# Performance work log

Hardware: AMD Instinct MI355X
Metric: run time of the kernel (lower is better)

## Reference

```python
import jax, jax.numpy as jnp
import numpy as np

N_HEADS = 32
N_KV_HEADS = 8
HEAD_DIM = 128
DIM = 4096
ROPE_THETA = 500000.0
BSZ, SEQLEN = 4, 1024


def _rope(t, cos, sin):
    # t: [B,S,H,hd]; cos/sin: [S,hd//2]
    te = t[..., 0::2]
    to = t[..., 1::2]
    c = cos[None, :, None, :]
    s = sin[None, :, None, :]
    out = jnp.stack([te * c - to * s, te * s + to * c], axis=-1)
    return out.reshape(t.shape)


def setup_inputs() -> dict:
    key = jax.random.key(0)
    ks = jax.random.split(key, 8)
    scale = 1.0 / np.sqrt(DIM)
    x = jax.random.normal(ks[0], (BSZ, SEQLEN, DIM), dtype=jnp.float32)
    wq = jax.random.normal(ks[1], (DIM, N_HEADS * HEAD_DIM), dtype=jnp.float32) * scale
    wk = jax.random.normal(ks[2], (DIM, N_KV_HEADS * HEAD_DIM), dtype=jnp.float32) * scale
    wv = jax.random.normal(ks[3], (DIM, N_KV_HEADS * HEAD_DIM), dtype=jnp.float32) * scale
    wo = jax.random.normal(ks[4], (N_HEADS * HEAD_DIM, DIM), dtype=jnp.float32) * scale
    # rotary tables: freqs_cis[s, j] = exp(i * s * theta^(-2j/hd))
    inv_freq = 1.0 / (ROPE_THETA ** (np.arange(0, HEAD_DIM, 2, dtype=np.float32) / HEAD_DIM))
    ang = np.outer(np.arange(SEQLEN, dtype=np.float32), inv_freq)
    freqs_cos = jnp.asarray(np.cos(ang), dtype=jnp.float32)
    freqs_sin = jnp.asarray(np.sin(ang), dtype=jnp.float32)
    # additive causal mask: 0 on/below diag, -inf above
    causal_mask = jnp.triu(jnp.full((SEQLEN, SEQLEN), -jnp.inf, dtype=jnp.float32), k=1)
    return {"x": x, "wq": wq, "wk": wk, "wv": wv, "wo": wo,
            "freqs_cos": freqs_cos, "freqs_sin": freqs_sin,
            "causal_mask": causal_mask, "fixed_point_iter": 0, "start_pos": 0}


def reference(x, wq, wk, wv, wo, freqs_cos, freqs_sin, causal_mask, fixed_point_iter, start_pos):
    B, S, _ = x.shape
    n_rep = N_HEADS // N_KV_HEADS
    xq = (x @ wq).reshape(B, S, N_HEADS, HEAD_DIM)
    xk = (x @ wk).reshape(B, S, N_KV_HEADS, HEAD_DIM)
    xv = (x @ wv).reshape(B, S, N_KV_HEADS, HEAD_DIM)
    xq = _rope(xq, freqs_cos, freqs_sin)
    xk = _rope(xk, freqs_cos, freqs_sin)
    # start_pos == 0 prefill: cache slice [:start_pos+S] equals freshly written xk/xv
    keys = jnp.repeat(xk, n_rep, axis=2)    # [B,S,H,hd]
    values = jnp.repeat(xv, n_rep, axis=2)
    scores = jnp.einsum('bqhd,bkhd->bhqk', xq, keys) / np.sqrt(HEAD_DIM)
    scores = scores + causal_mask  # broadcast [S,S]
    probs = jax.nn.softmax(scores.astype(jnp.float32), axis=-1).astype(xq.dtype)
    out = jnp.einsum('bhqk,bkhd->bqhd', probs, values)
    out = out.reshape(B, S, N_HEADS * HEAD_DIM)
    return out @ wo
```

## Files before the change

### kernel.cpp

```cpp
#include <hip/hip_runtime.h>

#define BSZ_  4
#define SEQ_  1024
#define NH_   32
#define NKVH_ 8
#define HD_   128
#define DIM_  4096
#define NTOK_ (BSZ_ * SEQ_)
#define QKVW_ 6144

typedef float  floatx4  __attribute__((ext_vector_type(4)));
typedef float  floatx16 __attribute__((ext_vector_type(16)));
typedef __bf16 bf16x8   __attribute__((ext_vector_type(8)));
typedef unsigned short ushortx8 __attribute__((ext_vector_type(8)));

__device__ __forceinline__ float fast_exp2(float x) {
  return __builtin_amdgcn_exp2f(x);
}

__device__ __forceinline__ unsigned short f2bf_bits(float f) {
  unsigned int u = __float_as_uint(f);
  u += 0x7FFFu + ((u >> 16) & 1u);
  return (unsigned short)(u >> 16);
}
__device__ __forceinline__ unsigned int pack_bf2_rne(float lo, float hi_) {
  return (unsigned int)f2bf_bits(lo) | ((unsigned int)f2bf_bits(hi_) << 16);
}
__device__ __forceinline__ unsigned int pack_bf2_trunc(float lo, float hi_) {
  return __builtin_amdgcn_perm(__float_as_uint(hi_), __float_as_uint(lo), 0x07060302u);
}

__device__ __forceinline__ void gld16(const void* g, void* l) {
  __builtin_amdgcn_global_load_lds(
      (const __attribute__((address_space(1))) void*)g,
      (__attribute__((address_space(3))) void*)l, 16, 0, 0);
}

__global__ __launch_bounds__(256)
void xconv(const float* __restrict__ X, unsigned short* __restrict__ XB)
{
  size_t i = ((size_t)blockIdx.x * 256 + threadIdx.x) * 4;
  float4 v = *(const float4*)&X[i];
  ushort4 o;
  o.x = f2bf_bits(v.x); o.y = f2bf_bits(v.y);
  o.z = f2bf_bits(v.z); o.w = f2bf_bits(v.w);
  *(ushort4*)&XB[i] = o;
}

__global__ __launch_bounds__(256)
void wtrans(const float* __restrict__ W, unsigned short* __restrict__ WT,
            int K, int N)
{
  __shared__ unsigned short T[32][36];
  const int k0 = blockIdx.y * 32, n0 = blockIdx.x * 32;
  const int t = threadIdx.x;
  {
    int kr = t >> 3, nc = (t & 7) * 4;
    float4 v = *(const float4*)&W[(size_t)(k0 + kr) * N + n0 + nc];
    T[kr][nc + 0] = f2bf_bits(v.x);
    T[kr][nc + 1] = f2bf_bits(v.y);
    T[kr][nc + 2] = f2bf_bits(v.z);
    T[kr][nc + 3] = f2bf_bits(v.w);
  }
  __syncthreads();
  {
    int nr = t >> 3, kc = (t & 7) * 4;
    ushort4 o;
    o.x = T[kc + 0][nr]; o.y = T[kc + 1][nr];
    o.z = T[kc + 2][nr]; o.w = T[kc + 3][nr];
    *(ushort4*)&WT[(size_t)(n0 + nr) * K + k0 + kc] = o;
  }
}

__global__ __launch_bounds__(256)
void vtrans2(const unsigned short* __restrict__ qkv, unsigned short* __restrict__ VT)
{
  __shared__ unsigned short T[32][36];
  const int bh = blockIdx.z;
  const int s0 = blockIdx.x * 32, d0 = blockIdx.y * 32;
  const int b = bh >> 3, kvh = bh & 7;
  const int t = threadIdx.x;
  {
    int sr = t >> 3, dc = (t & 7) * 4;
    ushort4 v = *(const ushort4*)&qkv[(size_t)(b * SEQ_ + s0 + sr) * QKVW_ + 5120 + kvh * HD_ + d0 + dc];
    T[sr][dc + 0] = v.x; T[sr][dc + 1] = v.y;
    T[sr][dc + 2] = v.z; T[sr][dc + 3] = v.w;
  }
  __syncthreads();
  {
    int dr = t >> 3, sc = (t & 7) * 4;
    ushort4 o;
    o.x = T[sc + 0][dr]; o.y = T[sc + 1][dr];
    o.z = T[sc + 2][dr]; o.w = T[sc + 3][dr];
    *(ushort4*)&VT[((size_t)bh * HD_ + d0 + dr) * SEQ_ + s0 + sc] = o;
  }
}

__global__ __launch_bounds__(256)
void rope2(unsigned int* __restrict__ t, const float* __restrict__ cosf,
           const float* __restrict__ sinf, int shift, int stride_u32, int base_u32)
{
  int idx = blockIdx.x * 256 + threadIdx.x;
  int tok = idx >> shift;
  int rem = idx & ((1 << shift) - 1);
  int d2  = idx & 63;
  int pos = tok & (SEQ_ - 1);
  unsigned int* p = &t[(size_t)tok * stride_u32 + base_u32 + rem];
  unsigned int pv = *p;
  float xe = __uint_as_float(pv << 16);
  float xo = __uint_as_float(pv & 0xFFFF0000u);
  float cv = cosf[pos * 64 + d2];
  float sv = sinf[pos * 64 + d2];
  float oe = xe * cv - xo * sv;
  float oo = xe * sv + xo * cv;
  *p = pack_bf2_rne(oe, oo);
}

template<bool OUT_BF16>
__global__ __launch_bounds__(512, 2)
void gemm_bt8(const unsigned short* __restrict__ A,
              const unsigned short* __restrict__ B,
              void* __restrict__ Cout, int M, int N, int K)
{
  __shared__ __align__(16) unsigned short As[4][256][32];
  __shared__ __align__(16) unsigned short Bs[4][256][32];

  const int tid  = threadIdx.x;
  const int w    = tid >> 6;
  const int lane = tid & 63;
  const int l16  = lane & 15;
  const int quad = lane >> 4;
  const int wr   = w >> 2;
  const int wc   = w & 3;

  int wg = blockIdx.x;
  const int q8 = gridDim.x >> 3;
  wg = (wg & 7) * q8 + (wg >> 3);
  const int nbx = N >> 8;
  const int bm = (wg / nbx) * 256;
  const int bn = (wg % nbx) * 256;

  const int srow     = w * 16 + (lane >> 2);
  const int cs_stage = (lane & 3) ^ ((srow >> 1) & 3);
  const int ntiles   = K >> 5;

  auto stageA = [&](int kt, int buf) {
#pragma unroll
    for (int r = 0; r < 2; r++)
      gld16(&A[(size_t)(bm + r * 128 + srow) * K + (kt << 5) + cs_stage * 8],
            (char*)&As[buf][0][0] + r * 8192 + w * 1024);
  };
  auto stageB = [&](int kt, int buf) {
#pragma unroll
    for (int r = 0; r < 2; r++)
      gld16(&B[(size_t)(bn + r * 128 + srow) * K + (kt << 5) + cs_stage * 8],
            (char*)&Bs[buf][0][0] + r * 8192 + w * 1024);
  };

  floatx4 acc[8][4];
#pragma unroll
  for (int i = 0; i < 8; i++)
#pragma unroll
    for (int j = 0; j < 4; j++) acc[i][j] = (floatx4){0.f, 0.f, 0.f, 0.f};

  const int sfrag = (l16 >> 1) & 3;
  const int cfr   = quad ^ sfrag;

#pragma unroll
  for (int t = 0; t < 3; t++) { stageA(t, t); stageB(t, t); }
  asm volatile("s_waitcnt vmcnt(8)" ::: "memory");
  __builtin_amdgcn_s_barrier();

  for (int t = 0; t < ntiles; t++) {
    const int buf  = t & 3;
    const int pbuf = (t + 3) & 3;
    const int pk   = (t + 3 < ntiles) ? (t + 3) : 0;
    const unsigned short* Ab = &As[buf][0][0];
    const unsigned short* Bb = &Bs[buf][0][0];

    bf16x8 bfr[4], af0[4], af1[4];
#pragma unroll
    for (int nj = 0; nj < 4; nj++)
      bfr[nj] = *(const bf16x8*)&Bb[(wc * 64 + nj * 16 + l16) * 32 + cfr * 8];
#pragma unroll
    for (int i = 0; i < 4; i++)
      af0[i] = *(const bf16x8*)&Ab[(wr * 128 + i * 16 + l16) * 32 + cfr * 8];
    stageA(pk, pbuf);
    __builtin_amdgcn_s_barrier();
    __builtin_amdgcn_s_setprio(1);
#pragma unroll
    for (int i = 0; i < 4; i++)
#pragma unroll
      for (int nj = 0; nj < 4; nj++)
        acc[i][nj] = __builtin_amdgcn_mfma_f32_16x16x32_bf16(af0[i], bfr[nj], acc[i][nj], 0, 0, 0);
    __builtin_amdgcn_s_setprio(0);
    __builtin_amdgcn_s_barrier();

#pragma unroll
    for (int i = 0; i < 4; i++)
      af1[i] = *(const bf16x8*)&Ab[(wr * 128 + (4 + i) * 16 + l16) * 32 + cfr * 8];
    stageB(pk, pbuf);
    __builtin_amdgcn_s_barrier();
    __builtin_amdgcn_s_setprio(1);
#pragma unroll
    for (int i = 0; i < 4; i++)
#pragma unroll
      for (int nj = 0; nj < 4; nj++)
        acc[4 + i][nj] = __builtin_amdgcn_mfma_f32_16x16x32_bf16(af1[i], bfr[nj], acc[4 + i][nj], 0, 0, 0);
    __builtin_amdgcn_s_setprio(0);
    asm volatile("s_waitcnt vmcnt(8)" ::: "memory");
    __builtin_amdgcn_s_barrier();
  }

#pragma unroll
  for (int mi = 0; mi < 8; mi++)
#pragma unroll
    for (int nj = 0; nj < 4; nj++)
#pragma unroll
      for (int r = 0; r < 4; r++) {
        size_t row = bm + wr * 128 + mi * 16 + quad * 4 + r;
        size_t col = bn + wc * 64 + nj * 16 + l16;
        if (OUT_BF16)
          ((unsigned short*)Cout)[row * N + col] = f2bf_bits(acc[mi][nj][r]);
        else
          ((float*)Cout)[row * N + col] = acc[mi][nj][r];
      }
}

__global__ __launch_bounds__(256, 2)
void flash_attn2(const unsigned short* __restrict__ qkv,
                 const unsigned short* __restrict__ vt,
                 unsigned short* __restrict__ o)
{
  __shared__ __align__(16) unsigned short S_[4][8192];
  unsigned short* Ks = &S_[0][0];
  unsigned short* Vs = &S_[1][0];

  const int bid = blockIdx.x;
  const int grp = bid >> 7;
  const int idx = bid & 127;
  const int qt = (grp == 0) ? 3 : (grp == 1) ? 2 : (grp == 2) ? 0 : 1;
  const int h = idx & 31, b = idx >> 5;

  const int kvh = h >> 2;
  const int tid = threadIdx.x, w = tid >> 6, lane = tid & 63;
  const int l31 = lane & 31, hi = lane >> 5;
  const int qb = qt * 256, qw = qb + w * 64;
  unsigned short* Ps = &S_[2][0] + w * 4096;

  const float CEXP = (float)(0.08838834764831845 * 1.4426950408889634);

  bf16x8 qf[2][8];
#pragma unroll
  for (int t2 = 0; t2 < 2; t2++) {
    const unsigned short* qrow =
        &qkv[(size_t)(b * SEQ_ + qw + t2 * 32 + l31) * QKVW_ + h * HD_ + hi * 8];
#pragma unroll
    for (int s = 0; s < 8; s++)
      qf[t2][s] = *(const bf16x8*)&qrow[s * 16];
  }

  floatx16 oa[2][4];
#pragma unroll
  for (int t2 = 0; t2 < 2; t2++)
#pragma unroll
    for (int dt = 0; dt < 4; dt++)
#pragma unroll
      for (int r = 0; r < 16; r++) oa[t2][dt][r] = 0.f;

  float ms[2] = {-3.0e38f, -3.0e38f};
  float ls[2] = {0.f, 0.f};

  const int nk = qb + 256;
  const int qmaxw = qw + 63;

  for (int kb_ = 0; kb_ < nk; kb_ += 64) {
    __syncthreads();
    {
      const size_t gbase = (size_t)(b * SEQ_ + kb_) * QKVW_ + 4096 + kvh * HD_;
#pragma unroll
      for (int it = 0; it < 4; it++) {
        int idx2 = it * 256 + tid;
        int key = idx2 >> 4, c = idx2 & 15;
        ushortx8 vld = *(const ushortx8*)&qkv[gbase + (size_t)key * QKVW_ + c * 8];
        *(ushortx8*)&Ks[key * 128 + ((c ^ (key & 15)) * 8)] = vld;
      }
      const size_t vbase = ((size_t)(b * NKVH_ + kvh) * HD_) * SEQ_ + kb_;
#pragma unroll
      for (int it = 0; it < 4; it++) {
        int idx2 = it * 256 + tid;
        int d = idx2 >> 3, c = idx2 & 7;
        ushortx8 vld = *(const ushortx8*)&vt[vbase + (size_t)d * SEQ_ + c * 8];
        *(ushortx8*)&Vs[d * 64 + ((c ^ (d & 7)) * 8)] = vld;
      }
    }
    __syncthreads();

    if (kb_ <= qmaxw) {
      const bool needmask = (kb_ + 63 > qw);

#pragma unroll
      for (int t2 = 0; t2 < 2; t2++) {
        floatx16 sc[2];
#pragma unroll
        for (int r = 0; r < 16; r++) { sc[0][r] = 0.f; sc[1][r] = 0.f; }
        __builtin_amdgcn_s_setprio(1);
#pragma unroll
        for (int s = 0; s < 8; s++) {
          int c = 2 * s + hi;
          bf16x8 k0 = *(const bf16x8*)&Ks[l31 * 128 + ((c ^ (l31 & 15)) * 8)];
          bf16x8 k1 = *(const bf16x8*)&Ks[(32 + l31) * 128 + ((c ^ ((32 + l31) & 15)) * 8)];
          sc[0] = __builtin_amdgcn_mfma_f32_32x32x16_bf16(k0, qf[t2][s], sc[0], 0, 0, 0);
          sc[1] = __builtin_amdgcn_mfma_f32_32x32x16_bf16(k1, qf[t2][s], sc[1], 0, 0, 0);
        }
        __builtin_amdgcn_s_setprio(0);

        if (needmask) {
          const int q = qw + t2 * 32 + l31;
#pragma unroll
          for (int k2 = 0; k2 < 2; k2++)
#pragma unroll
            for (int r = 0; r < 16; r++) {
              int key = kb_ + k2 * 32 + (r & 3) + 8 * (r >> 2) + 4 * hi;
              if (key > q) sc[k2][r] = -3.0e38f;
            }
        }

        float mx0 = sc[0][0], mx1 = sc[0][1];
#pragma unroll
        for (int r = 2; r < 16; r += 2) { mx0 = fmaxf(mx0, sc[0][r]); mx1 = fmaxf(mx1, sc[0][r + 1]); }
#pragma unroll
        for (int r = 0; r < 16; r += 2) { mx0 = fmaxf(mx0, sc[1][r]); mx1 = fmaxf(mx1, sc[1][r + 1]); }
        float mx = fmaxf(mx0, mx1);
        mx = fmaxf(mx, __shfl_xor(mx, 32));
        float mxs = mx * CEXP;
        float mn = fmaxf(ms[t2], mxs);
        float alpha = fast_exp2(ms[t2] - mn);
        ms[t2] = mn;

        float rs0 = 0.f, rs1 = 0.f;
        const int qloc = t2 * 32 + l31;
#pragma unroll
        for (int k2 = 0; k2 < 2; k2++) {
          unsigned int pk[8];
#pragma unroll
          for (int r = 0; r < 16; r += 2) {
            float p0 = fast_exp2(__builtin_fmaf(sc[k2][r],     CEXP, -mn));
            float p1 = fast_exp2(__builtin_fmaf(sc[k2][r + 1], CEXP, -mn));
            rs0 += p0; rs1 += p1;
            pk[r >> 1] = pack_bf2_trunc(p0, p1);
          }
#pragma unroll
          for (int rq = 0; rq < 4; rq++) {
            int keyoff = k2 * 32 + 8 * rq + 4 * hi;
            int c = keyoff >> 3;
            uint2 val = {pk[rq * 2], pk[rq * 2 + 1]};
            *(uint2*)&Ps[qloc * 64 + ((c ^ (qloc & 7)) * 8) + (keyoff & 7)] = val;
          }
        }
        float rs = rs0 + rs1;
        rs += __shfl_xor(rs, 32);
        ls[t2] = ls[t2] * alpha + rs;

        if (__any(alpha != 1.0f)) {
#pragma unroll
          for (int dt = 0; dt < 4; dt++)
#pragma unroll
            for (int r = 0; r < 16; r++) oa[t2][dt][r] *= alpha;
        }
      }

      __builtin_amdgcn_s_setprio(1);
#pragma unroll
      for (int ks = 0; ks < 4; ks++) {
        int c = 2 * ks + hi;
        bf16x8 pf0, pf1;
        {
          int q0l = l31;
          int q1l = 32 + l31;
          pf0 = *(const bf16x8*)&Ps[q0l * 64 + ((c ^ (q0l & 7)) * 8)];
          pf1 = *(const bf16x8*)&Ps[q1l * 64 + ((c ^ (q1l & 7)) * 8)];
        }
#pragma unroll
        for (int dt = 0; dt < 4; dt++) {
          int d = dt * 32 + l31;
          bf16x8 vf = *(const bf16x8*)&Vs[d * 64 + ((c ^ (d & 7)) * 8)];
          oa[0][dt] = __builtin_amdgcn_mfma_f32_32x32x16_bf16(vf, pf0, oa[0][dt], 0, 0, 0);
          oa[1][dt] = __builtin_amdgcn_mfma_f32_32x32x16_bf16(vf, pf1, oa[1][dt], 0, 0, 0);
        }
      }
      __builtin_amdgcn_s_setprio(0);
    }
  }

  __syncthreads();
  unsigned short* patch = &S_[w][0];
  float inv[2] = {1.0f / ls[0], 1.0f / ls[1]};
#pragma unroll
  for (int t2 = 0; t2 < 2; t2++) {
    const int qloc = t2 * 32 + l31;
#pragma unroll
    for (int dt = 0; dt < 4; dt++)
#pragma unroll
      for (int rq = 0; rq < 4; rq++) {
        float a0 = oa[t2][dt][rq * 4 + 0] * inv[t2];
        float a1 = oa[t2][dt][rq * 4 + 1] * inv[t2];
        float a2 = oa[t2][dt][rq * 4 + 2] * inv[t2];
        float a3 = oa[t2][dt][rq * 4 + 3] * inv[t2];
        int doff = dt * 32 + 8 * rq + 4 * hi;
        int c = doff >> 3;
        uint2 val = {pack_bf2_rne(a0, a1), pack_bf2_rne(a2, a3)};
        *(uint2*)&patch[qloc * 128 + ((c ^ (qloc & 7)) * 8) + (doff & 7)] = val;
      }
  }
#pragma unroll
  for (int it = 0; it < 16; it++) {
    int idx2 = it * 64 + lane;
    int row = idx2 >> 4, c = idx2 & 15;
    int cc = (c & 7) ^ (row & 7);
    int cs = (c & 8) | cc;
    ushortx8 vv = *(const ushortx8*)&patch[row * 128 + cs * 8];
    *(ushortx8*)&o[(size_t)(b * SEQ_ + qb + w * 64 + row) * 4096 + h * HD_ + c * 8] = vv;
  }
}

extern "C" void kernel_launch(void* const* d_in, const int* in_sizes, int n_in,
                              void* d_out, int out_size, void* d_ws, size_t ws_size,
                              hipStream_t stream)
{
  const float* x  = (const float*)d_in[0];
  const float* wq = (const float*)d_in[1];
  const float* wk = (const float*)d_in[2];
  const float* wv = (const float*)d_in[3];
  const float* wo = (const float*)d_in[4];
  const float* fc = (const float*)d_in[5];
  const float* fs = (const float*)d_in[6];
  float* out = (float*)d_out;

  unsigned short* xb    = (unsigned short*)d_ws;
  unsigned short* wqkvT = xb    + (size_t)NTOK_ * DIM_;
  unsigned short* qkvb  = wqkvT + (size_t)QKVW_ * DIM_;
  unsigned short* vtb   = qkvb  + (size_t)NTOK_ * QKVW_;
  unsigned short* ab    = xb;
  unsigned short* woT   = wqkvT;

  dim3 blk(256);

  xconv<<<(NTOK_ * DIM_ / 4) / 256, blk, 0, stream>>>(x, xb);
  wtrans<<<dim3(DIM_ / 32, DIM_ / 32), blk, 0, stream>>>(wq, wqkvT, DIM_, DIM_);
  wtrans<<<dim3((NKVH_ * HD_) / 32, DIM_ / 32), blk, 0, stream>>>(wk, wqkvT + (size_t)4096 * DIM_, DIM_, NKVH_ * HD_);
  wtrans<<<dim3((NKVH_ * HD_) / 32, DIM_ / 32), blk, 0, stream>>>(wv, wqkvT + (size_t)5120 * DIM_, DIM_, NKVH_ * HD_);

  gemm_bt8<true><<<dim3((QKVW_ / 256) * (NTOK_ / 256)), dim3(512), 0, stream>>>(
      xb, wqkvT, qkvb, NTOK_, QKVW_, DIM_);

  wtrans<<<dim3(DIM_ / 32, DIM_ / 32), blk, 0, stream>>>(wo, woT, DIM_, DIM_);

  rope2<<<(NTOK_ * 2048) / 256, blk, 0, stream>>>((unsigned int*)qkvb, fc, fs, 11, 3072, 0);
  rope2<<<(NTOK_ * 512) / 256, blk, 0, stream>>>((unsigned int*)qkvb, fc, fs, 9, 3072, 2048);

  vtrans2<<<dim3(SEQ_ / 32, HD_ / 32, BSZ_ * NKVH_), blk, 0, stream>>>(qkvb, vtb);

  flash_attn2<<<dim3((SEQ_ / 256) * NH_ * BSZ_), blk, 0, stream>>>(qkvb, vtb, ab);

  gemm_bt8<false><<<dim3((DIM_ / 256) * (NTOK_ / 256)), dim3(512), 0, stream>>>(
      ab, woT, out, NTOK_, DIM_, DIM_);
}
```

Before: 738.6 us.

## Prefetch next K/V tile into registers and skip lazy softmax rescale

The attention loop now loads the next 64-key K and V tile from global memory into registers while the current tile is being computed, then writes those registers to LDS at the top of the next iteration. This is meant to hide global load latency behind the MFMA work. It also adds a lazy online-softmax rescale: if every lane's new max is within 8 (exp2 units) of the running max, the max is left unchanged and alpha is 1, so the accumulator rescale is skipped. The prefetch raises register pressure, and the lazy rescale lets probabilities grow up to 2^8 before normalization, which bf16 and fp32 can absorb.

Measured after the change: 717.3 us. -2.9%, faster.

```diff
diff --git a/kernel.cpp b/kernel.cpp
--- a/kernel.cpp
+++ b/kernel.cpp
@@ -274,27 +274,43 @@
   const int nk = qb + 256;
   const int qmaxw = qw + 63;
 
+  ushortx8 kreg[4], vreg[4];
+  const size_t kg0 = (size_t)(b * SEQ_) * QKVW_ + 4096 + kvh * HD_;
+  const size_t vg0 = ((size_t)(b * NKVH_ + kvh) * HD_) * SEQ_;
+  const int krow = tid >> 4, kc = tid & 15;
+  const int vrow = tid >> 3, vc = tid & 7;
+
+  auto issue_loads = [&](int kb) {
+    const size_t gb = kg0 + (size_t)kb * QKVW_;
+#pragma unroll
+    for (int it = 0; it < 4; it++)
+      kreg[it] = *(const ushortx8*)&qkv[gb + (size_t)(it * 16 + krow) * QKVW_ + kc * 8];
+    const size_t vb = vg0 + kb;
+#pragma unroll
+    for (int it = 0; it < 4; it++)
+      vreg[it] = *(const ushortx8*)&vt[vb + (size_t)(it * 32 + vrow) * SEQ_ + vc * 8];
+  };
+  auto write_lds = [&]() {
+#pragma unroll
+    for (int it = 0; it < 4; it++) {
+      int key = it * 16 + krow;
+      *(ushortx8*)&Ks[key * 128 + ((kc ^ (key & 15)) * 8)] = kreg[it];
+    }
+#pragma unroll
+    for (int it = 0; it < 4; it++) {
+      int d = it * 32 + vrow;
+      *(ushortx8*)&Vs[d * 64 + ((vc ^ (d & 7)) * 8)] = vreg[it];
+    }
+  };
+
+  issue_loads(0);
+
   for (int kb_ = 0; kb_ < nk; kb_ += 64) {
     __syncthreads();
-    {
-      const size_t gbase = (size_t)(b * SEQ_ + kb_) * QKVW_ + 4096 + kvh * HD_;
-#pragma unroll
-      for (int it = 0; it < 4; it++) {
-        int idx2 = it * 256 + tid;
-        int key = idx2 >> 4, c = idx2 & 15;
-        ushortx8 vld = *(const ushortx8*)&qkv[gbase + (size_t)key * QKVW_ + c * 8];
-        *(ushortx8*)&Ks[key * 128 + ((c ^ (key & 15)) * 8)] = vld;
-      }
-      const size_t vbase = ((size_t)(b * NKVH_ + kvh) * HD_) * SEQ_ + kb_;
-#pragma unroll
-      for (int it = 0; it < 4; it++) {
-        int idx2 = it * 256 + tid;
-        int d = idx2 >> 3, c = idx2 & 7;
-        ushortx8 vld = *(const ushortx8*)&vt[vbase + (size_t)d * SEQ_ + c * 8];
-        *(ushortx8*)&Vs[d * 64 + ((c ^ (d & 7)) * 8)] = vld;
-      }
-    }
-    __syncthreads();
+    write_lds();
+    if (kb_ + 64 < nk) issue_loads(kb_ + 64);
+    asm volatile("s_waitcnt lgkmcnt(0)" ::: "memory");
+    __builtin_amdgcn_s_barrier();
 
     if (kb_ <= qmaxw) {
       const bool needmask = (kb_ + 63 > qw);
@@ -334,9 +350,15 @@
         float mx = fmaxf(mx0, mx1);
         mx = fmaxf(mx, __shfl_xor(mx, 32));
         float mxs = mx * CEXP;
-        float mn = fmaxf(ms[t2], mxs);
-        float alpha = fast_exp2(ms[t2] - mn);
-        ms[t2] = mn;
+
+        float mn, alpha;
+        if (__all(mxs - ms[t2] <= 8.0f)) {
+          mn = ms[t2]; alpha = 1.0f;
+        } else {
+          mn = fmaxf(ms[t2], mxs);
+          alpha = fast_exp2(ms[t2] - mn);
+          ms[t2] = mn;
+        }
 
         float rs0 = 0.f, rs1 = 0.f;
         const int qloc = t2 * 32 + l31;
```
